# Optimization experiments

Measured on AMD Instinct MI355X. Metric: run time of the kernel, lower is better.

The kernel has to match this reference:

```python
import jax, jax.numpy as jnp
import numpy as np

WS = 8      # window size
NH = 8      # num heads
DIM = 128   # channels


def _rel_index(ws):
    # Swin relative-position index, identical to the torch buffer construction
    coords = np.stack(np.meshgrid(np.arange(ws), np.arange(ws), indexing='ij')).reshape(2, -1)
    rel = (coords[:, :, None] - coords[:, None, :]).transpose(1, 2, 0)  # [N,N,2]
    rel[:, :, 0] += ws - 1
    rel[:, :, 1] += ws - 1
    rel[:, :, 0] *= 2 * ws - 1
    return rel.sum(-1)  # [N,N] in [0, (2ws-1)^2)


def setup_inputs() -> dict:
    key = jax.random.key(0)
    ks = jax.random.split(key, 4)
    return {
        'x': jax.random.normal(ks[0], (2, DIM, 256, 256), jnp.float32),
        'qkv_w': jax.random.normal(ks[1], (3 * DIM, DIM), jnp.float32) * 0.02,
        'qkv_b': jnp.zeros((3 * DIM,), jnp.float32),
        'proj_w': jax.random.normal(ks[2], (DIM, DIM), jnp.float32) * 0.02,
        'proj_b': jnp.zeros((DIM,), jnp.float32),
        'rel_bias': jax.random.normal(ks[3], ((2 * WS - 1) ** 2, NH), jnp.float32) * 0.02,
        'rel_index': jnp.asarray(_rel_index(WS), jnp.int32),
    }


def reference(x, qkv_w, qkv_b, proj_w, proj_b, rel_bias, rel_index):
    B, C, H, W = x.shape
    ws, nh = WS, NH
    hd = C // nh
    scale = hd ** -0.5
    pad_h = (-H) % ws
    pad_w = (-W) % ws
    x = jnp.pad(x, ((0, 0), (0, 0), (0, pad_h), (0, pad_w)))
    Hp, Wp = H + pad_h, W + pad_w
    N = ws * ws
    # window partition -> tokens [B*nWh*nWw, N, C] (channels-last; 1x1 conv == linear)
    xw = x.reshape(B, C, Hp // ws, ws, Wp // ws, ws)
    xw = xw.transpose(0, 2, 4, 3, 5, 1).reshape(-1, N, C)
    qkv = xw @ qkv_w.T + qkv_b                      # [Bw, N, 3C]
    q, k, v = jnp.split(qkv, 3, axis=-1)

    def heads(t):  # [Bw, N, C] -> [Bw, nh, N, hd]
        return t.reshape(t.shape[0], N, nh, hd).transpose(0, 2, 1, 3)

    q, k, v = heads(q), heads(k), heads(v)
    attn = jnp.einsum('bhid,bhjd->bhij', q, k) * scale   # [Bw, nh, N, N]
    bias = rel_bias[rel_index].transpose(2, 0, 1)        # [nh, N, N]
    attn = jax.nn.softmax(attn + bias[None], axis=-1)
    out = jnp.einsum('bhij,bhjd->bhid', attn, v)         # [Bw, nh, N, hd]
    out = out.transpose(0, 2, 1, 3).reshape(-1, N, C)    # [Bw, N, C]
    # window un-partition -> [B, C, Hp, Wp]
    out = out.reshape(B, Hp // ws, Wp // ws, ws, ws, C)
    out = out.transpose(0, 5, 1, 3, 2, 4).reshape(B, C, Hp, Wp)
    out = out[:, :, :H, :W]
    # proj: 1x1 conv
    return jnp.einsum('bchw,oc->bohw', out, proj_w) + proj_b[None, :, None, None]
```

## Files before the change

### kernel.cpp

```cpp
#include <hip/hip_runtime.h>

#define CDIM 128
#define NHEADS 8
#define HD 16
#define NTOK 64
#define HW 65536
#define XSTR 136
#define VSTR 72
#define LOG2E 1.44269504088896f

typedef short s8v __attribute__((ext_vector_type(8)));
typedef short s4v __attribute__((ext_vector_type(4)));
typedef float f4v __attribute__((ext_vector_type(4)));

static __device__ __forceinline__ short f2bf(float f) {
    unsigned u = __float_as_uint(f);
    u += 0x7FFFu + ((u >> 16) & 1u);
    return (short)(u >> 16);
}

__global__ __launch_bounds__(256) void pack_w_kernel(
    const float* __restrict__ qkv_w, const float* __restrict__ proj_w,
    short* __restrict__ wpk)
{
    int idx = blockIdx.x * 256 + threadIdx.x;
    int lane = idx & 63, kc = (idx >> 6) & 3, ob = idx >> 8;
    int row = (ob < 24) ? ob * 16 + (lane & 15) : (ob - 24) * 16 + (lane & 15);
    int col = kc * 32 + (lane >> 4) * 8;
    const float* src = ((ob < 24) ? qkv_w : proj_w) + (size_t)row * CDIM + col;
    float sc = (ob < 8) ? 0.25f * LOG2E : 1.0f;
    float4 f0 = *(const float4*)src;
    float4 f1 = *(const float4*)(src + 4);
    s8v r;
    r[0] = f2bf(f0.x * sc); r[1] = f2bf(f0.y * sc);
    r[2] = f2bf(f0.z * sc); r[3] = f2bf(f0.w * sc);
    r[4] = f2bf(f1.x * sc); r[5] = f2bf(f1.y * sc);
    r[6] = f2bf(f1.z * sc); r[7] = f2bf(f1.w * sc);
    *(s8v*)&wpk[(size_t)idx * 8] = r;
}

__global__ __launch_bounds__(256) void pack_b_kernel(
    const float* __restrict__ rel_bias, const int* __restrict__ rel_index,
    float* __restrict__ biasf)
{
    int idx = blockIdx.x * 256 + threadIdx.x;
    int lane = idx & 63, nt = (idx >> 6) & 3, mq = (idx >> 8) & 3, h = idx >> 10;
    int tq  = mq * 16 + (lane & 15);
    int tk0 = nt * 16 + (lane >> 4) * 4;
    f4v v;
    #pragma unroll
    for (int r = 0; r < 4; ++r)
        v[r] = LOG2E * rel_bias[rel_index[tq * 64 + tk0 + r] * NHEADS + h];
    *(f4v*)&biasf[(size_t)idx * 4] = v;
}

__global__ __launch_bounds__(256, 3) void winattn_kernel(
    const float* __restrict__ x, const float* __restrict__ qkv_b,
    const float* __restrict__ proj_b, const short* __restrict__ wpk,
    const float* __restrict__ biasf, float* __restrict__ out)
{
    __shared__ __align__(16) short xs[NTOK * XSTR];
    __shared__ __align__(16) short ks[NTOK * XSTR];
    __shared__ __align__(16) short vsc[4 * 2 * 16 * VSTR];

    const int tid  = threadIdx.x;
    const int lane = tid & 63;
    const int wv   = tid >> 6;
    const int qd   = lane >> 4;
    const int l15  = lane & 15;

    const int wid = (blockIdx.x & 7) * 256 + (blockIdx.x >> 3);
    const int b   = wid >> 10;
    const int wy  = (wid >> 5) & 31, wx = wid & 31;
    const int h0  = wy * 8, w0 = wx * 8;
    const float* xb = x + (size_t)b * CDIM * HW;

    #pragma unroll
    for (int it = 0; it < 8; ++it) {
        const int g   = it * 4 + wv;
        const int cg  = g & 15, tqg = g >> 4;
        const int c   = cg * 8 + (lane & 7);
        const int tq  = tqg * 8 + ((lane >> 3) & 7);
        const int t0  = tq * 4;
        float4 f = *(const float4*)&xb[(size_t)c * HW + (h0 + (t0 >> 3)) * 256 + w0 + (t0 & 7)];
        const int col = ((cg ^ (tq & 7)) << 3) | (c & 7);
        xs[(t0 + 0) * XSTR + col] = f2bf(f.x);
        xs[(t0 + 1) * XSTR + col] = f2bf(f.y);
        xs[(t0 + 2) * XSTR + col] = f2bf(f.z);
        xs[(t0 + 3) * XSTR + col] = f2bf(f.w);
    }
    __syncthreads();

    s8v vf[2][2];
    {
        s8v X[4][4];
        #pragma unroll
        for (int tb = 0; tb < 4; ++tb)
            #pragma unroll
            for (int kc = 0; kc < 4; ++kc) {
                const int gr = ((4 * kc + qd) ^ ((4 * tb + (l15 >> 2)) & 7)) << 3;
                X[tb][kc] = *(const s8v*)&xs[(tb * 16 + l15) * XSTR + gr];
            }

        const s8v* wf = (const s8v*)wpk;

        {
            s8v Wk[2][4];
            #pragma unroll
            for (int hp = 0; hp < 2; ++hp) {
                const int ob = 8 + wv + hp * 4;
                #pragma unroll
                for (int kc = 0; kc < 4; ++kc) Wk[hp][kc] = wf[(ob * 4 + kc) * 64 + lane];
            }
            #pragma unroll
            for (int hp = 0; hp < 2; ++hp) {
                const int h = wv + hp * 4;
                float4 kb = *(const float4*)&qkv_b[128 + h * 16 + qd * 4];
                float kbr[4] = {kb.x, kb.y, kb.z, kb.w};
                #pragma unroll
                for (int tb = 0; tb < 4; ++tb) {
                    f4v acc = {0.f, 0.f, 0.f, 0.f};
                    #pragma unroll
                    for (int kc = 0; kc < 4; ++kc)
                        acc = __builtin_amdgcn_mfma_f32_16x16x32_bf16(Wk[hp][kc], X[tb][kc], acc, 0, 0, 0);
                    s4v pk;
                    #pragma unroll
                    for (int r = 0; r < 4; ++r) pk[r] = f2bf(acc[r] + kbr[r]);
                    *(s4v*)&ks[(tb * 16 + l15) * XSTR + h * 16 + qd * 4] = pk;
                }
            }
        }

        {
            s8v Wv[2][4];
            #pragma unroll
            for (int hp = 0; hp < 2; ++hp) {
                const int ob = 16 + wv + hp * 4;
                #pragma unroll
                for (int kc = 0; kc < 4; ++kc) Wv[hp][kc] = wf[(ob * 4 + kc) * 64 + lane];
            }
            #pragma unroll
            for (int hp = 0; hp < 2; ++hp) {
                const int h = wv + hp * 4;
                short* vw = &vsc[(wv * 2 + hp) * 16 * VSTR];
                const float vb = qkv_b[256 + h * 16 + l15];
                #pragma unroll
                for (int tb = 0; tb < 4; ++tb) {
                    f4v acc = {0.f, 0.f, 0.f, 0.f};
                    #pragma unroll
                    for (int kc = 0; kc < 4; ++kc)
                        acc = __builtin_amdgcn_mfma_f32_16x16x32_bf16(X[tb][kc], Wv[hp][kc], acc, 0, 0, 0);
                    s4v pk;
                    #pragma unroll
                    for (int r = 0; r < 4; ++r) pk[r] = f2bf(acc[r] + vb);
                    *(s4v*)&vw[l15 * VSTR + tb * 16 + qd * 4] = pk;
                }
                vf[hp][0] = *(const s8v*)&vw[l15 * VSTR + qd * 8];
                vf[hp][1] = *(const s8v*)&vw[l15 * VSTR + 32 + qd * 8];
            }
        }

        s8v Wq[2][4];
        #pragma unroll
        for (int hp = 0; hp < 2; ++hp) {
            const int ob = wv + hp * 4;
            #pragma unroll
            for (int kc = 0; kc < 4; ++kc) Wq[hp][kc] = wf[(ob * 4 + kc) * 64 + lane];
        }

        __syncthreads();

        #pragma unroll
        for (int hp = 0; hp < 2; ++hp) {
            const int h = wv + hp * 4;
            float4 qb = *(const float4*)&qkv_b[h * 16 + qd * 4];
            const float qsc = 0.25f * LOG2E;
            float qbr[4] = {qb.x * qsc, qb.y * qsc, qb.z * qsc, qb.w * qsc};
            #pragma unroll
            for (int tb = 0; tb < 4; ++tb) {
                f4v acc = {0.f, 0.f, 0.f, 0.f};
                #pragma unroll
                for (int kc = 0; kc < 4; ++kc)
                    acc = __builtin_amdgcn_mfma_f32_16x16x32_bf16(Wq[hp][kc], X[tb][kc], acc, 0, 0, 0);
                s4v pk;
                #pragma unroll
                for (int r = 0; r < 4; ++r) pk[r] = f2bf(acc[r] + qbr[r]);
                *(s4v*)&xs[(tb * 16 + l15) * XSTR + h * 16 + qd * 4] = pk;
            }
        }
    }

    short* os = xs;
    const s8v z8 = {};
    s8v kf[2][4];
    #pragma unroll
    for (int hp = 0; hp < 2; ++hp) {
        const int h = wv + hp * 4;
        #pragma unroll
        for (int nt = 0; nt < 4; ++nt) {
            s8v kr = *(const s8v*)&ks[(nt * 16 + l15) * XSTR + h * 16 + (qd & 1) * 8];
            kf[hp][nt] = (qd < 2) ? kr : z8;
        }
    }
    #pragma unroll
    for (int mq = 0; mq < 4; ++mq) {
        f4v bf[2][4];
        #pragma unroll
        for (int hp = 0; hp < 2; ++hp) {
            const int h = wv + hp * 4;
            #pragma unroll
            for (int nt = 0; nt < 4; ++nt)
                bf[hp][nt] = *(const f4v*)&biasf[(size_t)(((h * 4 + mq) * 4 + nt) * 64 + lane) * 4];
        }
        s8v qf[2];
        #pragma unroll
        for (int hp = 0; hp < 2; ++hp) {
            const int h = wv + hp * 4;
            qf[hp] = *(const s8v*)&xs[(mq * 16 + l15) * XSTR + h * 16 + (qd & 1) * 8];
        }
        f4v sv[2][4];
        #pragma unroll
        for (int hp = 0; hp < 2; ++hp)
            #pragma unroll
            for (int nt = 0; nt < 4; ++nt) {
                f4v s = {0.f, 0.f, 0.f, 0.f};
                s = __builtin_amdgcn_mfma_f32_16x16x32_bf16(kf[hp][nt], qf[hp], s, 0, 0, 0);
                sv[hp][nt] = s + bf[hp][nt];
            }
        float mx[2];
        #pragma unroll
        for (int hp = 0; hp < 2; ++hp) {
            f4v a01, a23, a;
            #pragma unroll
            for (int r = 0; r < 4; ++r) {
                a01[r] = fmaxf(sv[hp][0][r], sv[hp][1][r]);
                a23[r] = fmaxf(sv[hp][2][r], sv[hp][3][r]);
            }
            #pragma unroll
            for (int r = 0; r < 4; ++r) a[r] = fmaxf(a01[r], a23[r]);
            float m = fmaxf(fmaxf(a[0], a[1]), fmaxf(a[2], a[3]));
            m = fmaxf(m, __shfl_xor(m, 16, 64));
            m = fmaxf(m, __shfl_xor(m, 32, 64));
            mx[hp] = m;
        }
        float inv[2];
        #pragma unroll
        for (int hp = 0; hp < 2; ++hp) {
            #pragma unroll
            for (int nt = 0; nt < 4; ++nt)
                #pragma unroll
                for (int r = 0; r < 4; ++r)
                    sv[hp][nt][r] = exp2f(sv[hp][nt][r] - mx[hp]);
            f4v s01 = sv[hp][0] + sv[hp][1];
            f4v s23 = sv[hp][2] + sv[hp][3];
            f4v s4  = s01 + s23;
            float sm = (s4[0] + s4[1]) + (s4[2] + s4[3]);
            sm += __shfl_xor(sm, 16, 64);
            sm += __shfl_xor(sm, 32, 64);
            inv[hp] = 1.f / sm;
        }
        #pragma unroll
        for (int hp = 0; hp < 2; ++hp) {
            const int h = wv + hp * 4;
            short* pw = &vsc[(wv * 2 + hp) * 16 * VSTR];
            #pragma unroll
            for (int nt = 0; nt < 4; ++nt) {
                s4v pk;
                #pragma unroll
                for (int r = 0; r < 4; ++r) pk[r] = f2bf(sv[hp][nt][r] * inv[hp]);
                *(s4v*)&pw[l15 * VSTR + nt * 16 + qd * 4] = pk;
            }
            s8v pa0 = *(const s8v*)&pw[l15 * VSTR + qd * 8];
            s8v pa1 = *(const s8v*)&pw[l15 * VSTR + 32 + qd * 8];
            f4v O = {0.f, 0.f, 0.f, 0.f};
            O = __builtin_amdgcn_mfma_f32_16x16x32_bf16(pa0, vf[hp][0], O, 0, 0, 0);
            O = __builtin_amdgcn_mfma_f32_16x16x32_bf16(pa1, vf[hp][1], O, 0, 0, 0);
            #pragma unroll
            for (int r = 0; r < 4; ++r)
                os[(mq * 16 + qd * 4 + r) * XSTR + h * HD + l15] = f2bf(O[r]);
        }
    }

    const s8v* wf = (const s8v*)wpk;
    s8v B[2][4];
    float pb2[2]; int o2[2];
    #pragma unroll
    for (int nt = 0; nt < 2; ++nt) {
        const int ob = 24 + wv * 2 + nt;
        o2[nt] = (wv * 2 + nt) * 16 + l15;
        pb2[nt] = proj_b[o2[nt]];
        #pragma unroll
        for (int kc = 0; kc < 4; ++kc) B[nt][kc] = wf[(ob * 4 + kc) * 64 + lane];
    }
    __syncthreads();
    {
        s8v A[4][4];
        #pragma unroll
        for (int mt = 0; mt < 4; ++mt)
            #pragma unroll
            for (int kc = 0; kc < 4; ++kc)
                A[mt][kc] = *(const s8v*)&xs[(mt * 16 + l15) * XSTR + kc * 32 + qd * 8];

        #pragma unroll
        for (int mt = 0; mt < 4; ++mt) {
            const int t0 = mt * 16 + qd * 4;
            const int pix = (h0 + (t0 >> 3)) * 256 + w0 + (t0 & 7);
            #pragma unroll
            for (int nt = 0; nt < 2; ++nt) {
                f4v acc = {0.f, 0.f, 0.f, 0.f};
                #pragma unroll
                for (int kc = 0; kc < 4; ++kc)
                    acc = __builtin_amdgcn_mfma_f32_16x16x32_bf16(A[mt][kc], B[nt][kc], acc, 0, 0, 0);
                float4 v = make_float4(acc[0] + pb2[nt], acc[1] + pb2[nt],
                                       acc[2] + pb2[nt], acc[3] + pb2[nt]);
                *(float4*)&out[((size_t)(b * CDIM + o2[nt])) * HW + pix] = v;
            }
        }
    }
}

extern "C" void kernel_launch(void* const* d_in, const int* in_sizes, int n_in,
                              void* d_out, int out_size, void* d_ws, size_t ws_size,
                              hipStream_t stream) {
    const float* x        = (const float*)d_in[0];
    const float* qkv_w    = (const float*)d_in[1];
    const float* qkv_b    = (const float*)d_in[2];
    const float* proj_w   = (const float*)d_in[3];
    const float* proj_b   = (const float*)d_in[4];
    const float* rel_bias = (const float*)d_in[5];
    const int*   rel_index= (const int*)d_in[6];
    float* out = (float*)d_out;

    short* wpk   = (short*)d_ws;
    float* biasf = (float*)((char*)d_ws + 131072);

    pack_w_kernel<<<32, 256, 0, stream>>>(qkv_w, proj_w, wpk);
    pack_b_kernel<<<32, 256, 0, stream>>>(rel_bias, rel_index, biasf);
    winattn_kernel<<<2048, 256, 0, stream>>>(x, qkv_b, proj_b, wpk, biasf, out);
}
```

Measured before the change: 168.7 us.

## Drop shared K buffer, store K per-wave swizzled, use packed bf16 converts

Removes the block-wide K shared array and stores each wave's K heads in its own swizzled per-wave slot, reusing the V/P scratch region. This cuts LDS use so occupancy can rise from 3 to 4 blocks per CU. The software bf16 rounding is replaced with the hardware v_cvt_pk_bf16_f32 instruction, and the x-load lane mapping is changed for different coalescing and bank behaviour. The tighter register bound may force spills, and K reads now rely on the per-wave swizzle being correct.

```diff
diff --git a/kernel.cpp b/kernel.cpp
--- a/kernel.cpp
+++ b/kernel.cpp
@@ -7,6 +7,8 @@
 #define HW 65536
 #define XSTR 136
 #define VSTR 72
+#define KST 16
+#define SLOT 2304
 #define LOG2E 1.44269504088896f
 
 typedef short s8v __attribute__((ext_vector_type(8)));
@@ -17,6 +19,14 @@
     unsigned u = __float_as_uint(f);
     u += 0x7FFFu + ((u >> 16) & 1u);
     return (short)(u >> 16);
+}
+static __device__ __forceinline__ unsigned cvt2(float lo, float hi) {
+    unsigned r;
+    asm("v_cvt_pk_bf16_f32 %0, %1, %2" : "=v"(r) : "v"(lo), "v"(hi));
+    return r;
+}
+static __device__ __forceinline__ uint2 pk4(float a, float b, float c, float d) {
+    return make_uint2(cvt2(a, b), cvt2(c, d));
 }
 
 __global__ __launch_bounds__(256) void pack_w_kernel(
@@ -54,20 +64,20 @@
     *(f4v*)&biasf[(size_t)idx * 4] = v;
 }
 
-__global__ __launch_bounds__(256, 3) void winattn_kernel(
+__global__ __launch_bounds__(256, 4) void winattn_kernel(
     const float* __restrict__ x, const float* __restrict__ qkv_b,
     const float* __restrict__ proj_b, const short* __restrict__ wpk,
     const float* __restrict__ biasf, float* __restrict__ out)
 {
     __shared__ __align__(16) short xs[NTOK * XSTR];
-    __shared__ __align__(16) short ks[NTOK * XSTR];
-    __shared__ __align__(16) short vsc[4 * 2 * 16 * VSTR];
+    __shared__ __align__(16) short vsc[4 * SLOT];
 
     const int tid  = threadIdx.x;
     const int lane = tid & 63;
     const int wv   = tid >> 6;
     const int qd   = lane >> 4;
     const int l15  = lane & 15;
+    short* myv = &vsc[wv * SLOT];
 
     const int wid = (blockIdx.x & 7) * 256 + (blockIdx.x >> 3);
     const int b   = wid >> 10;
@@ -79,8 +89,8 @@
     for (int it = 0; it < 8; ++it) {
         const int g   = it * 4 + wv;
         const int cg  = g & 15, tqg = g >> 4;
-        const int c   = cg * 8 + (lane & 7);
-        const int tq  = tqg * 8 + ((lane >> 3) & 7);
+        const int c   = cg * 8 + ((lane >> 3) & 7);
+        const int tq  = tqg * 8 + (lane & 7);
         const int t0  = tq * 4;
         float4 f = *(const float4*)&xb[(size_t)c * HW + (h0 + (t0 >> 3)) * 256 + w0 + (t0 & 7)];
         const int col = ((cg ^ (tq & 7)) << 3) | (c & 7);
@@ -92,6 +102,8 @@
     __syncthreads();
 
     s8v vf[2][2];
+    s8v kf[2][4];
+    const int kswz = (l15 >> 1) & 2;
     {
         s8v X[4][4];
         #pragma unroll
@@ -104,59 +116,44 @@
 
         const s8v* wf = (const s8v*)wpk;
 
-        {
-            s8v Wk[2][4];
-            #pragma unroll
-            for (int hp = 0; hp < 2; ++hp) {
-                const int ob = 8 + wv + hp * 4;
-                #pragma unroll
-                for (int kc = 0; kc < 4; ++kc) Wk[hp][kc] = wf[(ob * 4 + kc) * 64 + lane];
-            }
-            #pragma unroll
-            for (int hp = 0; hp < 2; ++hp) {
-                const int h = wv + hp * 4;
-                float4 kb = *(const float4*)&qkv_b[128 + h * 16 + qd * 4];
-                float kbr[4] = {kb.x, kb.y, kb.z, kb.w};
-                #pragma unroll
-                for (int tb = 0; tb < 4; ++tb) {
-                    f4v acc = {0.f, 0.f, 0.f, 0.f};
-                    #pragma unroll
-                    for (int kc = 0; kc < 4; ++kc)
-                        acc = __builtin_amdgcn_mfma_f32_16x16x32_bf16(Wk[hp][kc], X[tb][kc], acc, 0, 0, 0);
-                    s4v pk;
-                    #pragma unroll
-                    for (int r = 0; r < 4; ++r) pk[r] = f2bf(acc[r] + kbr[r]);
-                    *(s4v*)&ks[(tb * 16 + l15) * XSTR + h * 16 + qd * 4] = pk;
-                }
-            }
-        }
-
-        {
-            s8v Wv[2][4];
-            #pragma unroll
-            for (int hp = 0; hp < 2; ++hp) {
-                const int ob = 16 + wv + hp * 4;
-                #pragma unroll
-                for (int kc = 0; kc < 4; ++kc) Wv[hp][kc] = wf[(ob * 4 + kc) * 64 + lane];
-            }
-            #pragma unroll
-            for (int hp = 0; hp < 2; ++hp) {
-                const int h = wv + hp * 4;
-                short* vw = &vsc[(wv * 2 + hp) * 16 * VSTR];
-                const float vb = qkv_b[256 + h * 16 + l15];
-                #pragma unroll
-                for (int tb = 0; tb < 4; ++tb) {
-                    f4v acc = {0.f, 0.f, 0.f, 0.f};
-                    #pragma unroll
-                    for (int kc = 0; kc < 4; ++kc)
-                        acc = __builtin_amdgcn_mfma_f32_16x16x32_bf16(X[tb][kc], Wv[hp][kc], acc, 0, 0, 0);
-                    s4v pk;
-                    #pragma unroll
-                    for (int r = 0; r < 4; ++r) pk[r] = f2bf(acc[r] + vb);
-                    *(s4v*)&vw[l15 * VSTR + tb * 16 + qd * 4] = pk;
-                }
-                vf[hp][0] = *(const s8v*)&vw[l15 * VSTR + qd * 8];
-                vf[hp][1] = *(const s8v*)&vw[l15 * VSTR + 32 + qd * 8];
+        #pragma unroll
+        for (int hp = 0; hp < 2; ++hp) {
+            const int h = wv + hp * 4;
+            const int ob = 16 + h;
+            s8v Wv[4];
+            #pragma unroll
+            for (int kc = 0; kc < 4; ++kc) Wv[kc] = wf[(ob * 4 + kc) * 64 + lane];
+            short* vw = myv + hp * 16 * VSTR;
+            const float vb = qkv_b[256 + h * 16 + l15];
+            #pragma unroll
+            for (int tb = 0; tb < 4; ++tb) {
+                f4v acc = {0.f, 0.f, 0.f, 0.f};
+                #pragma unroll
+                for (int kc = 0; kc < 4; ++kc)
+                    acc = __builtin_amdgcn_mfma_f32_16x16x32_bf16(X[tb][kc], Wv[kc], acc, 0, 0, 0);
+                *(uint2*)&vw[l15 * VSTR + tb * 16 + qd * 4] =
+                    pk4(acc[0] + vb, acc[1] + vb, acc[2] + vb, acc[3] + vb);
+            }
+            vf[hp][0] = *(const s8v*)&vw[l15 * VSTR + qd * 8];
+            vf[hp][1] = *(const s8v*)&vw[l15 * VSTR + 32 + qd * 8];
+        }
+
+        #pragma unroll
+        for (int hp = 0; hp < 2; ++hp) {
+            const int h = wv + hp * 4;
+            const int ob = 8 + h;
+            s8v Wk[4];
+            #pragma unroll
+            for (int kc = 0; kc < 4; ++kc) Wk[kc] = wf[(ob * 4 + kc) * 64 + lane];
+            float4 kb = *(const float4*)&qkv_b[128 + h * 16 + qd * 4];
+            #pragma unroll
+            for (int tb = 0; tb < 4; ++tb) {
+                f4v acc = {0.f, 0.f, 0.f, 0.f};
+                #pragma unroll
+                for (int kc = 0; kc < 4; ++kc)
+                    acc = __builtin_amdgcn_mfma_f32_16x16x32_bf16(Wk[kc], X[tb][kc], acc, 0, 0, 0);
+                *(uint2*)&myv[((hp * 64 + tb * 16 + l15) << 4) + ((qd ^ kswz) << 2)] =
+                    pk4(acc[0] + kb.x, acc[1] + kb.y, acc[2] + kb.z, acc[3] + kb.w);
             }
         }
 
@@ -175,33 +172,30 @@
             const int h = wv + hp * 4;
             float4 qb = *(const float4*)&qkv_b[h * 16 + qd * 4];
             const float qsc = 0.25f * LOG2E;
-            float qbr[4] = {qb.x * qsc, qb.y * qsc, qb.z * qsc, qb.w * qsc};
             #pragma unroll
             for (int tb = 0; tb < 4; ++tb) {
                 f4v acc = {0.f, 0.f, 0.f, 0.f};
                 #pragma unroll
                 for (int kc = 0; kc < 4; ++kc)
                     acc = __builtin_amdgcn_mfma_f32_16x16x32_bf16(Wq[hp][kc], X[tb][kc], acc, 0, 0, 0);
-                s4v pk;
-                #pragma unroll
-                for (int r = 0; r < 4; ++r) pk[r] = f2bf(acc[r] + qbr[r]);
-                *(s4v*)&xs[(tb * 16 + l15) * XSTR + h * 16 + qd * 4] = pk;
-            }
-        }
+                *(uint2*)&xs[(tb * 16 + l15) * XSTR + h * 16 + qd * 4] =
+                    pk4(acc[0] + qb.x * qsc, acc[1] + qb.y * qsc,
+                        acc[2] + qb.z * qsc, acc[3] + qb.w * qsc);
+            }
+        }
+
+        const s8v z8 = {};
+        #pragma unroll
+        for (int hp = 0; hp < 2; ++hp)
+            #pragma unroll
+            for (int nt = 0; nt < 4; ++nt) {
+                s8v kr = *(const s8v*)&myv[((hp * 64 + nt * 16 + l15) << 4) +
+                                           (((2 * (qd & 1)) ^ kswz) << 2)];
+                kf[hp][nt] = (qd < 2) ? kr : z8;
+            }
     }
 
     short* os = xs;
-    const s8v z8 = {};
-    s8v kf[2][4];
-    #pragma unroll
-    for (int hp = 0; hp < 2; ++hp) {
-        const int h = wv + hp * 4;
-        #pragma unroll
-        for (int nt = 0; nt < 4; ++nt) {
-            s8v kr = *(const s8v*)&ks[(nt * 16 + l15) * XSTR + h * 16 + (qd & 1) * 8];
-            kf[hp][nt] = (qd < 2) ? kr : z8;
-        }
-    }
     #pragma unroll
     for (int mq = 0; mq < 4; ++mq) {
         f4v bf[2][4];
@@ -262,14 +256,12 @@
         #pragma unroll
         for (int hp = 0; hp < 2; ++hp) {
             const int h = wv + hp * 4;
-            short* pw = &vsc[(wv * 2 + hp) * 16 * VSTR];
-            #pragma unroll
-            for (int nt = 0; nt < 4; ++nt) {
-                s4v pk;
-                #pragma unroll
-                for (int r = 0; r < 4; ++r) pk[r] = f2bf(sv[hp][nt][r] * inv[hp]);
-                *(s4v*)&pw[l15 * VSTR + nt * 16 + qd * 4] = pk;
-            }
+            short* pw = myv + hp * 16 * VSTR;
+            #pragma unroll
+            for (int nt = 0; nt < 4; ++nt)
+                *(uint2*)&pw[l15 * VSTR + nt * 16 + qd * 4] =
+                    pk4(sv[hp][nt][0] * inv[hp], sv[hp][nt][1] * inv[hp],
+                        sv[hp][nt][2] * inv[hp], sv[hp][nt][3] * inv[hp]);
             s8v pa0 = *(const s8v*)&pw[l15 * VSTR + qd * 8];
             s8v pa1 = *(const s8v*)&pw[l15 * VSTR + 32 + qd * 8];
             f4v O = {0.f, 0.f, 0.f, 0.f};
```

New measurement: 181.5 us. 7.6% more time.
